# Kernel optimization log

Measured on AMD Instinct MI355X. Metric: run time of the kernel, lower is better.

The kernel has to match this reference:

```python
import jax, jax.numpy as jnp
import numpy as np

K = 20
EPS = 1e-5

def leaky(y):
    return jnp.where(y > 0, y, 0.2 * y)

def knn(x, k):
    # x: [B, C, N] -> idx [B, N, k] of nearest neighbors (incl. self)
    xx = jnp.sum(x * x, axis=1)                      # [B, N]
    inner = jnp.einsum('bcn,bcm->bnm', x, x)          # [B, N, N]
    pd = -xx[:, :, None] + 2.0 * inner - xx[:, None, :]  # negative sq dist
    return jax.lax.top_k(pd, k)[1]

def get_graph_feature(x, k):
    # x: [B, C, N] -> [B, 2C, N, k]
    idx = knn(x, k)
    xt = jnp.transpose(x, (0, 2, 1))                  # [B, N, C]
    feat = jax.vmap(lambda xb, ib: xb[ib])(xt, idx)   # [B, N, k, C]
    center = xt[:, :, None, :]
    out = jnp.concatenate([feat - center, jnp.broadcast_to(center, feat.shape)], axis=-1)
    return jnp.transpose(out, (0, 3, 1, 2))

def bn(y, g, b, axes, shape):
    m = jnp.mean(y, axis=axes, keepdims=True)
    v = jnp.var(y, axis=axes, keepdims=True)
    return (y - m) * jax.lax.rsqrt(v + EPS) * g.reshape(shape) + b.reshape(shape)

def edge_block(x, W, g, b, k):
    f = get_graph_feature(x, k)                       # [B, 2C, N, k]
    y = jnp.einsum('bcnk,oc->bonk', f, W)             # 1x1 conv2d, no bias
    y = leaky(bn(y, g, b, (0, 2, 3), (1, -1, 1, 1)))
    return jnp.max(y, axis=-1)                        # [B, O, N]

def setup_inputs():
    key = jax.random.key(0)
    ks = jax.random.split(key, 8)
    d = {
        'x':  jax.random.normal(ks[0], (16, 3, 2048), jnp.float32),
        'W1': jax.random.normal(ks[1], (64, 6), jnp.float32) * 0.1,
        'g1': jnp.ones((64,)), 'b1': jnp.zeros((64,)),
        'W2': jax.random.normal(ks[2], (64, 128), jnp.float32) * 0.1,
        'g2': jnp.ones((64,)), 'b2': jnp.zeros((64,)),
        'W3': jax.random.normal(ks[3], (128, 128), jnp.float32) * 0.1,
        'g3': jnp.ones((128,)), 'b3': jnp.zeros((128,)),
        'W4': jax.random.normal(ks[4], (256, 256), jnp.float32) * 0.1,
        'g4': jnp.ones((256,)), 'b4': jnp.zeros((256,)),
        'W5': jax.random.normal(ks[5], (1024, 512), jnp.float32) * 0.05,
        'g5': jnp.ones((1024,)), 'b5': jnp.zeros((1024,)),
        'Wl': jax.random.normal(ks[6], (256, 2048), jnp.float32) * 0.02,
        'g6': jnp.ones((256,)), 'b6': jnp.zeros((256,)),
    }
    return d

def reference(x, W1, g1, b1, W2, g2, b2, W3, g3, b3, W4, g4, b4, W5, g5, b5, Wl, g6, b6):
    x1 = edge_block(x,  W1, g1, b1, K)   # [B, 64, N]
    x2 = edge_block(x1, W2, g2, b2, K)   # [B, 64, N]
    x3 = edge_block(x2, W3, g3, b3, K)   # [B, 128, N]
    x4 = edge_block(x3, W4, g4, b4, K)   # [B, 256, N]
    h = jnp.concatenate([x1, x2, x3, x4], axis=1)       # [B, 512, N]
    y = jnp.einsum('bcn,oc->bon', h, W5)                 # 1x1 conv1d
    y = leaky(bn(y, g5, b5, (0, 2), (1, -1, 1)))         # [B, 1024, N]
    p = jnp.concatenate([jnp.max(y, axis=-1), jnp.mean(y, axis=-1)], axis=1)  # [B, 2048]
    z = p @ Wl.T                                          # [B, 256]
    return bn(z, g6, b6, (0,), (1, -1))
```

## Files before the change

kernel.cpp:

```cpp
#include <hip/hip_runtime.h>
#include <float.h>
#include <math.h>

#define BB 16
#define NN 2048
#define KNNK 20
#define HC 512
#define O5 1024
#define EPSF 1e-5f
#define GBLK 2048

__device__ __forceinline__ float leakyf(float y){ return y > 0.f ? y : 0.2f*y; }

__device__ __forceinline__ void bsort_step(float& v, int& id, int lane, int k, int j){
  float pv = __shfl_xor(v, j, 64);
  int pid = __shfl_xor(id, j, 64);
  bool up = ((lane & k) == 0);
  bool iLow = ((lane & j) == 0);
  bool pBefore = (pv > v) || (pv == v && pid < id);
  if ((up == iLow) ? pBefore : !pBefore){ v = pv; id = pid; }
}

__global__ void k_transpose(const float* __restrict__ x, float* __restrict__ xP){
  int gid = blockIdx.x*256 + threadIdx.x;
  if (gid >= BB*NN) return;
  int b = gid / NN, n = gid % NN;
  const float* xb = x + (size_t)b*3*NN;
  *(float4*)&xP[(size_t)gid*4] = make_float4(xb[n], xb[NN + n], xb[2*NN + n], 0.f);
}

__global__ void k_sqn(const float* __restrict__ xin, int xs, int C, float* __restrict__ sqn){
  int gid = blockIdx.x*256 + threadIdx.x;
  if (gid >= BB*NN) return;
  const float* r = xin + (size_t)gid*xs;
  float s = 0.f;
  for (int c = 0; c < C; ++c){ float v = r[c]; s = fmaf(v, v, s); }
  sqn[gid] = s;
}

template<int C, bool WARM>
__global__ __launch_bounds__(256) void k_knn(const float* __restrict__ xin, int xs,
                                             const float* __restrict__ sqn,
                                             const int* __restrict__ idx_prev,
                                             int* __restrict__ idx_out){
  const int TN = 16, MC = 256;
  __shared__ float xnT[WARM ? 1 : 8][20];
  __shared__ float xmT[(C == 3 ? 1 : 16)][MC + 4];
  __shared__ float cval[TN][24];
  __shared__ int   cidx[TN][24];
  __shared__ float sqnn[TN];
  int tid = threadIdx.x;
  int b = (blockIdx.x*TN) / NN, n0 = (blockIdx.x*TN) % NN;
  const float* xb = xin + (size_t)b*NN*xs;

  if constexpr (!WARM){
    for (int e = tid; e < TN*C; e += 256){
      int r = e / C, c = e % C;
      xnT[c][r] = xb[(size_t)(n0+r)*xs + c];
    }
  }
  if (tid < TN) sqnn[tid] = sqn[b*NN + n0 + tid];
  __syncthreads();

  int wid = tid >> 6, lane = tid & 63, r0 = wid*4;
  float tv[4]; int ti[4];

  int urow[4];
  #pragma unroll
  for (int i = 0; i < 4; ++i) urow[i] = __builtin_amdgcn_readfirstlane(n0 + r0 + i);

  if constexpr (WARM){
    #pragma unroll
    for (int i = 0; i < 4; ++i){
      int r = r0 + i;
      int m = (lane < KNNK) ? idx_prev[(size_t)(b*NN + n0 + r)*KNNK + lane] : 0;
      const float* xq = xb + (size_t)urow[i]*xs;
      const float* xm = xb + (size_t)m*xs;
      float dot = 0.f;
      #pragma unroll 8
      for (int c = 0; c < C; c += 4){
        float4 qv = *(const float4*)(xq + c);
        float4 mv = *(const float4*)(xm + c);
        dot = fmaf(qv.x, mv.x, dot);
        dot = fmaf(qv.y, mv.y, dot);
        dot = fmaf(qv.z, mv.z, dot);
        dot = fmaf(qv.w, mv.w, dot);
      }
      float dval = (lane < KNNK) ? ((2.f*dot - sqnn[r]) - sqn[b*NN + m]) : -FLT_MAX;
      int did = (lane < KNNK) ? m : 0x7fffffff;
      #pragma unroll
      for (int k = 2; k <= 64; k <<= 1)
        #pragma unroll
        for (int jj = k >> 1; jj > 0; jj >>= 1)
          bsort_step(dval, did, lane, k, jj);
      if (lane < KNNK){ cval[r][lane] = dval; cidx[r][lane] = did; }
      tv[i] = __shfl(dval, KNNK-1); ti[i] = __shfl(did, KNNK-1);
    }
    __syncthreads();
  }

  for (int base = 0; base < NN; base += MC){
    float pd[4][4];
    if constexpr (C == 3){
      int m0g = base + lane*4;
      const float* xm = xb + (size_t)m0g*4;
      float4 q0 = *(const float4*)&xm[0];
      float4 q1 = *(const float4*)&xm[4];
      float4 q2 = *(const float4*)&xm[8];
      float4 q3 = *(const float4*)&xm[12];
      float4 sm4 = *(const float4*)&sqn[b*NN + m0g];
      #pragma unroll
      for (int i = 0; i < 4; ++i){
        float a0 = xnT[0][r0+i], a1 = xnT[1][r0+i], a2 = xnT[2][r0+i], sq = sqnn[r0+i];
        float d0 = a0*q0.x; d0 = fmaf(a1, q0.y, d0); d0 = fmaf(a2, q0.z, d0);
        float d1 = a0*q1.x; d1 = fmaf(a1, q1.y, d1); d1 = fmaf(a2, q1.z, d1);
        float d2 = a0*q2.x; d2 = fmaf(a1, q2.y, d2); d2 = fmaf(a2, q2.z, d2);
        float d3 = a0*q3.x; d3 = fmaf(a1, q3.y, d3); d3 = fmaf(a2, q3.z, d3);
        pd[i][0] = (2.f*d0 - sq) - sm4.x;
        pd[i][1] = (2.f*d1 - sq) - sm4.y;
        pd[i][2] = (2.f*d2 - sq) - sm4.z;
        pd[i][3] = (2.f*d3 - sq) - sm4.w;
      }
    } else {
      float acc[4][4] = {};
      const float* xq0 = xb + (size_t)urow[0]*xs;
      const float* xq1 = xb + (size_t)urow[1]*xs;
      const float* xq2 = xb + (size_t)urow[2]*xs;
      const float* xq3 = xb + (size_t)urow[3]*xs;
      int pm = tid >> 2, fq = tid & 3;
      for (int c0 = 0; c0 < C; c0 += 16){
        #pragma unroll
        for (int p = 0; p < 4; ++p){
          int pt = p*64 + pm;
          float4 vv = *(const float4*)(xb + (size_t)(base + pt)*xs + c0 + fq*4);
          xmT[fq*4+0][pt] = vv.x; xmT[fq*4+1][pt] = vv.y;
          xmT[fq*4+2][pt] = vv.z; xmT[fq*4+3][pt] = vv.w;
        }
        __syncthreads();
        #pragma unroll
        for (int cc4 = 0; cc4 < 16; cc4 += 4){
          float aq[4][4];
          *(float4*)&aq[0][0] = *(const float4*)(xq0 + c0 + cc4);
          *(float4*)&aq[1][0] = *(const float4*)(xq1 + c0 + cc4);
          *(float4*)&aq[2][0] = *(const float4*)(xq2 + c0 + cc4);
          *(float4*)&aq[3][0] = *(const float4*)(xq3 + c0 + cc4);
          #pragma unroll
          for (int dc = 0; dc < 4; ++dc){
            float4 m4 = *(const float4*)&xmT[cc4+dc][lane*4];
            float mv[4] = {m4.x, m4.y, m4.z, m4.w};
            #pragma unroll
            for (int i = 0; i < 4; ++i)
              #pragma unroll
              for (int p = 0; p < 4; ++p)
                acc[i][p] = fmaf(aq[i][dc], mv[p], acc[i][p]);
          }
        }
        __syncthreads();
      }
      float4 sm4 = *(const float4*)&sqn[b*NN + base + lane*4];
      float smr[4] = {sm4.x, sm4.y, sm4.z, sm4.w};
      #pragma unroll
      for (int i = 0; i < 4; ++i){
        float sq = sqnn[r0+i];
        #pragma unroll
        for (int j = 0; j < 4; ++j)
          pd[i][j] = (2.f*acc[i][j] - sq) - smr[j];
      }
    }

    bool handled = false;
    if constexpr (!WARM){
      if (base == 0){
        handled = true;
        float lv[4]; int li[4];
        #pragma unroll
        for (int i = 0; i < 4; ++i){
          float v0 = pd[i][0]; int j0 = 0;
          if (pd[i][1] > v0){ v0 = pd[i][1]; j0 = 1; }
          if (pd[i][2] > v0){ v0 = pd[i][2]; j0 = 2; }
          if (pd[i][3] > v0){ v0 = pd[i][3]; j0 = 3; }
          lv[i] = v0; li[i] = lane*4 + j0;
        }
        float bv[4]; int bi[4];
        for (int it = 0; it < KNNK; ++it){
          #pragma unroll
          for (int i = 0; i < 4; ++i){ bv[i] = lv[i]; bi[i] = li[i]; }
          #pragma unroll
          for (int off = 1; off < 64; off <<= 1){
            #pragma unroll
            for (int i = 0; i < 4; ++i){
              float ov = __shfl_xor(bv[i], off, 64);
              int oi = __shfl_xor(bi[i], off, 64);
              if (ov > bv[i] || (ov == bv[i] && oi < bi[i])){ bv[i] = ov; bi[i] = oi; }
            }
          }
          #pragma unroll
          for (int i = 0; i < 4; ++i){
            if (lane == it){ cval[r0+i][it] = bv[i]; cidx[r0+i][it] = bi[i]; }
            int wl = bi[i] >> 2, wj = bi[i] & 3;
            if (lane == wl){
              pd[i][0] = (wj == 0) ? -FLT_MAX : pd[i][0];
              pd[i][1] = (wj == 1) ? -FLT_MAX : pd[i][1];
              pd[i][2] = (wj == 2) ? -FLT_MAX : pd[i][2];
              pd[i][3] = (wj == 3) ? -FLT_MAX : pd[i][3];
              float v0 = pd[i][0]; int j0 = 0;
              if (pd[i][1] > v0){ v0 = pd[i][1]; j0 = 1; }
              if (pd[i][2] > v0){ v0 = pd[i][2]; j0 = 2; }
              if (pd[i][3] > v0){ v0 = pd[i][3]; j0 = 3; }
              lv[i] = v0; li[i] = lane*4 + j0;
            }
          }
        }
        #pragma unroll
        for (int i = 0; i < 4; ++i){ tv[i] = bv[i]; ti[i] = bi[i]; }
      }
    }
    if (!handled){
      #pragma unroll
      for (int i = 0; i < 4; ++i){
        int r = r0 + i;
        bool pred = false;
        #pragma unroll
        for (int j = 0; j < 4; ++j){
          int ci = base + lane*4 + j;
          pred = pred || (pd[i][j] > tv[i]) || (pd[i][j] == tv[i] && ci < ti[i]);
        }
        unsigned long long mask = __ballot(pred);
        while (mask){
          int l = __builtin_ctzll(mask); mask &= (mask - 1);
          float cv0 = __shfl(pd[i][0], l);
          float cv1 = __shfl(pd[i][1], l);
          float cv2 = __shfl(pd[i][2], l);
          float cv3 = __shfl(pd[i][3], l);
          #pragma unroll
          for (int j = 0; j < 4; ++j){
            float cv = (j == 0) ? cv0 : (j == 1) ? cv1 : (j == 2) ? cv2 : cv3;
            int ci = base + l*4 + j;
            if (cv > tv[i] || (cv == tv[i] && ci < ti[i])){
              bool skip = false;
              if constexpr (WARM){
                skip = __ballot((lane < KNNK) && (cidx[r][lane] == ci)) != 0ull;
              }
              if (!skip){
                float ev = -FLT_MAX; int ei = 0x7fffffff;
                if (lane < KNNK){ ev = cval[r][lane]; ei = cidx[r][lane]; }
                bool ahead = (lane < KNNK) && (ev > cv || (ev == cv && ei < ci));
                int pos = __popcll(__ballot(ahead));
                float pev = __shfl_up(ev, 1);
                int   pei = __shfl_up(ei, 1);
                float nv; int ni;
                if (lane < pos){ nv = ev; ni = ei; }
                else if (lane == pos){ nv = cv; ni = ci; }
                else { nv = pev; ni = pei; }
                if (lane < KNNK){ cval[r][lane] = nv; cidx[r][lane] = ni; }
                tv[i] = __shfl(nv, 19); ti[i] = __shfl(ni, 19);
              }
            }
          }
        }
      }
    }
  }

  if (lane < KNNK){
    #pragma unroll
    for (int i = 0; i < 4; ++i){
      int r = r0 + i;
      idx_out[(size_t)(b*NN + n0 + r)*KNNK + lane] = cidx[r][lane];
    }
  }
}

__global__ void k_wprep(const float* __restrict__ W, int O, int C,
                        float* __restrict__ wu, float* __restrict__ wv){
  int i = blockIdx.x*256 + threadIdx.x;
  if (i >= O*C) return;
  int o = i / C, c = i % C;
  float a = W[(size_t)o*2*C + c], b = W[(size_t)o*2*C + C + c];
  wu[i] = a; wv[i] = b - a;
}

__global__ __launch_bounds__(256) void k_uv(const float* __restrict__ xin, int xs, int C,
                                            const float* __restrict__ wu, const float* __restrict__ wv,
                                            int O, float* __restrict__ u, float* __restrict__ v){
  __shared__ float xsh[16][68];
  __shared__ float wush[16][68], wvsh[16][68];
  int tid = threadIdx.x;
  int rb = blockIdx.x*64, ob = blockIdx.y*64;
  int otx = tid % 16, rty = tid / 16;
  float au[4][4] = {}, av[4][4] = {};
  for (int c0 = 0; c0 < C; c0 += 16){
    #pragma unroll
    for (int i = 0; i < 4; ++i){
      int c = otx, r = rty*4 + i;
      xsh[c][r]  = (c0 + c < C) ? xin[(size_t)(rb+r)*xs + c0 + c] : 0.f;
      wush[c][r] = (c0 + c < C) ? wu[(size_t)(ob+r)*C + c0 + c] : 0.f;
      wvsh[c][r] = (c0 + c < C) ? wv[(size_t)(ob+r)*C + c0 + c] : 0.f;
    }
    __syncthreads();
    #pragma unroll
    for (int c = 0; c < 16; ++c){
      float4 xr = *(const float4*)&xsh[c][rty*4];
      float4 wa = *(const float4*)&wush[c][otx*4];
      float4 wb = *(const float4*)&wvsh[c][otx*4];
      float xv[4] = {xr.x, xr.y, xr.z, xr.w};
      float wav[4] = {wa.x, wa.y, wa.z, wa.w};
      float wbv[4] = {wb.x, wb.y, wb.z, wb.w};
      #pragma unroll
      for (int i = 0; i < 4; ++i)
        #pragma unroll
        for (int j = 0; j < 4; ++j){
          au[i][j] = fmaf(xv[i], wav[j], au[i][j]);
          av[i][j] = fmaf(xv[i], wbv[j], av[i][j]);
        }
    }
    __syncthreads();
  }
  #pragma unroll
  for (int i = 0; i < 4; ++i){
    size_t r = (size_t)(rb + rty*4 + i);
    *(float4*)&u[r*O + ob + otx*4] = make_float4(au[i][0], au[i][1], au[i][2], au[i][3]);
    *(float4*)&v[r*O + ob + otx*4] = make_float4(av[i][0], av[i][1], av[i][2], av[i][3]);
  }
}

__global__ __launch_bounds__(256) void k_gather(const float* __restrict__ u, const float* __restrict__ v,
                                                const int* __restrict__ idx, int O,
                                                float* __restrict__ s,
                                                float* __restrict__ gp1, float* __restrict__ gp2){
  __shared__ float r1[256], r2[256];
  int tid = threadIdx.x;
  int Ppar = 256 / O;
  int o = tid % O, g = tid / O;
  int p0 = blockIdx.x*16;
  float cs = 0.f, cs2 = 0.f;
  int IT = 16 / Ppar;
  for (int it = 0; it < IT; ++it){
    int pi = p0 + it*Ppar + g;
    int b = pi / NN;
    const int* il = idx + (size_t)pi*KNNK;
    float vv = v[(size_t)pi*O + o];
    float mx = -FLT_MAX, su = 0.f, su2 = 0.f;
    #pragma unroll
    for (int k = 0; k < KNNK; ++k){
      int m = il[k];
      float um = u[((size_t)b*NN + m)*O + o];
      mx = fmaxf(mx, um); su += um; su2 = fmaf(um, um, su2);
    }
    s[(size_t)pi*O + o] = mx + vv;
    cs += su + (float)KNNK*vv;
    cs2 += su2 + 2.f*vv*su + (float)KNNK*vv*vv;
  }
  r1[tid] = cs; r2[tid] = cs2;
  __syncthreads();
  if (tid < O){
    float t1 = 0.f, t2 = 0.f;
    for (int gg = 0; gg < Ppar; ++gg){ t1 += r1[gg*O + tid]; t2 += r2[gg*O + tid]; }
    gp1[(size_t)tid*GBLK + blockIdx.x] = t1;
    gp2[(size_t)tid*GBLK + blockIdx.x] = t2;
  }
}

__global__ __launch_bounds__(256) void k_pred(const float* __restrict__ gp1, const float* __restrict__ gp2,
                                              float* __restrict__ S1, float* __restrict__ S2){
  __shared__ float r1[256], r2[256];
  int o = blockIdx.x, t = threadIdx.x;
  float a = 0.f, b = 0.f;
  #pragma unroll
  for (int i = 0; i < GBLK/256; ++i){
    a += gp1[(size_t)o*GBLK + i*256 + t];
    b += gp2[(size_t)o*GBLK + i*256 + t];
  }
  r1[t] = a; r2[t] = b;
  __syncthreads();
  for (int off = 128; off > 0; off >>= 1){
    if (t < off){ r1[t] += r1[t + off]; r2[t] += r2[t + off]; }
    __syncthreads();
  }
  if (t == 0){ S1[o] = r1[0]; S2[o] = r2[0]; }
}

__global__ void k_fin(const float* __restrict__ S1, const float* __restrict__ S2,
                      const float* __restrict__ g, const float* __restrict__ bb,
                      int O, float cnt, float* __restrict__ A, float* __restrict__ Bp){
  int o = blockIdx.x*256 + threadIdx.x;
  if (o >= O) return;
  float m = S1[o] / cnt;
  float var = S2[o] / cnt - m*m;
  float sc = g[o] / sqrtf(var + EPSF);
  A[o] = sc; Bp[o] = bb[o] - m*sc;
}

__global__ void k_bnle(const float* __restrict__ s, const float* __restrict__ A,
                       const float* __restrict__ Bp, int O, int choff, float* __restrict__ h){
  int gid = blockIdx.x*256 + threadIdx.x;
  int row = gid / O, o = gid % O;
  h[(size_t)row*HC + choff + o] = leakyf(fmaf(s[gid], A[o], Bp[o]));
}

__global__ void k_colsum(const float* __restrict__ hh, float* __restrict__ cp){
  __shared__ float red[4][64];
  int c = threadIdx.x & 63, g = threadIdx.x >> 6;
  int cb = blockIdx.x*64;
  int rbase = blockIdx.y*2048;
  float sacc = 0.f;
  for (int r = rbase + g; r < rbase + 2048; r += 4)
    sacc += hh[(size_t)r*HC + cb + c];
  red[g][c] = sacc;
  __syncthreads();
  if (threadIdx.x < 64){
    float t = red[0][c] + red[1][c] + red[2][c] + red[3][c];
    cp[(size_t)blockIdx.y*HC + cb + c] = t;
  }
}

__global__ void k_csred(const float* __restrict__ cp, float* __restrict__ cs){
  int c = blockIdx.x*256 + threadIdx.x;
  if (c >= HC) return;
  float s = 0.f;
  for (int g = 0; g < 16; ++g) s += cp[(size_t)g*HC + c];
  cs[c] = s;
}

__global__ __launch_bounds__(256) void k_syrk(const float* __restrict__ hh, float* __restrict__ Gp){
  __shared__ float as[16][132], bs[16][132];
  int tid = threadIdx.x;
  int ib = blockIdx.x*128, jb = blockIdx.y*128;
  int k0 = blockIdx.z*1024;
  int cx = tid & 15, ry = tid >> 4;
  int skk = tid >> 4, scc = (tid & 15)*8;
  float acc[8][8] = {};
  for (int kk0 = k0; kk0 < k0 + 1024; kk0 += 16){
    {
      const float* ra = &hh[(size_t)(kk0 + skk)*HC + ib + scc];
      const float* rb2 = &hh[(size_t)(kk0 + skk)*HC + jb + scc];
      float4 a0 = *(const float4*)ra, a1 = *(const float4*)(ra + 4);
      float4 b0 = *(const float4*)rb2, b1 = *(const float4*)(rb2 + 4);
      *(float4*)&as[skk][scc] = a0; *(float4*)&as[skk][scc+4] = a1;
      *(float4*)&bs[skk][scc] = b0; *(float4*)&bs[skk][scc+4] = b1;
    }
    __syncthreads();
    #pragma unroll
    for (int kk = 0; kk < 16; ++kk){
      float4 a0 = *(const float4*)&as[kk][ry*8];
      float4 a1 = *(const float4*)&as[kk][ry*8+4];
      float4 b0 = *(const float4*)&bs[kk][cx*8];
      float4 b1 = *(const float4*)&bs[kk][cx*8+4];
      float av[8] = {a0.x,a0.y,a0.z,a0.w,a1.x,a1.y,a1.z,a1.w};
      float bv[8] = {b0.x,b0.y,b0.z,b0.w,b1.x,b1.y,b1.z,b1.w};
      #pragma unroll
      for (int i = 0; i < 8; ++i)
        #pragma unroll
        for (int j = 0; j < 8; ++j)
          acc[i][j] = fmaf(av[i], bv[j], acc[i][j]);
    }
    __syncthreads();
  }
  float* gz = Gp + (size_t)blockIdx.z*HC*HC;
  #pragma unroll
  for (int i = 0; i < 8; ++i){
    size_t row = (size_t)(ib + ry*8 + i);
    *(float4*)&gz[row*HC + jb + cx*8]     = make_float4(acc[i][0], acc[i][1], acc[i][2], acc[i][3]);
    *(float4*)&gz[row*HC + jb + cx*8 + 4] = make_float4(acc[i][4], acc[i][5], acc[i][6], acc[i][7]);
  }
}

__global__ void k_gred(const float* __restrict__ Gp, float* __restrict__ G){
  int e = blockIdx.x*256 + threadIdx.x;
  float s = 0.f;
  for (int z = 0; z < 32; ++z) s += Gp[(size_t)z*HC*HC + e];
  G[e] = s;
}

__global__ __launch_bounds__(256) void k_quad(const float* __restrict__ G, const float* __restrict__ W5,
                                              const float* __restrict__ cs,
                                              float* __restrict__ S1, float* __restrict__ S2){
  __shared__ float wsh[512];
  __shared__ float red[256];
  int o = blockIdx.x, tid = threadIdx.x;
  for (int j = tid; j < 512; j += 256) wsh[j] = W5[(size_t)o*HC + j];
  __syncthreads();
  float q = 0.f;
  for (int i = tid; i < 512; i += 256){
    float wi = wsh[i];
    float rd = 0.f;
    for (int j = 0; j < 512; j += 4){
      float4 gv = *(const float4*)&G[(size_t)i*HC + j];
      rd = fmaf(gv.x, wsh[j], rd); rd = fmaf(gv.y, wsh[j+1], rd);
      rd = fmaf(gv.z, wsh[j+2], rd); rd = fmaf(gv.w, wsh[j+3], rd);
    }
    q = fmaf(wi, rd, q);
  }
  float m = 0.f;
  for (int j = tid; j < 512; j += 256) m = fmaf(wsh[j], cs[j], m);
  red[tid] = q; __syncthreads();
  for (int off = 128; off > 0; off >>= 1){ if (tid < off) red[tid] += red[tid + off]; __syncthreads(); }
  if (tid == 0) S2[o] = red[0];
  __syncthreads();
  red[tid] = m; __syncthreads();
  for (int off = 128; off > 0; off >>= 1){ if (tid < off) red[tid] += red[tid + off]; __syncthreads(); }
  if (tid == 0) S1[o] = red[0];
}

__global__ __launch_bounds__(256) void k_gemm5b(const float* __restrict__ hh, const float* __restrict__ W5,
                                                const float* __restrict__ A, const float* __restrict__ Bp,
                                                float* __restrict__ mpart, float* __restrict__ spart){
  __shared__ float hs[16][132];
  __shared__ float ws[16][132];
  int tid = threadIdx.x;
  int rb = blockIdx.x*128, ob = blockIdx.y*128;
  int cx = tid & 15, ry = tid >> 4;
  float acc[8][8] = {};
  for (int c0 = 0; c0 < 512; c0 += 16){
    int rr = tid & 127, q0 = (tid >> 7)*4;
    #pragma unroll
    for (int qq = 0; qq < 2; ++qq){
      int kk = q0 + qq*8;
      float4 hv = *(const float4*)&hh[(size_t)(rb+rr)*HC + c0 + kk];
      hs[kk+0][rr] = hv.x; hs[kk+1][rr] = hv.y; hs[kk+2][rr] = hv.z; hs[kk+3][rr] = hv.w;
      float4 wv = *(const float4*)&W5[(size_t)(ob+rr)*HC + c0 + kk];
      ws[kk+0][rr] = wv.x; ws[kk+1][rr] = wv.y; ws[kk+2][rr] = wv.z; ws[kk+3][rr] = wv.w;
    }
    __syncthreads();
    #pragma unroll
    for (int kk = 0; kk < 16; ++kk){
      float4 a0 = *(const float4*)&hs[kk][ry*8];
      float4 a1 = *(const float4*)&hs[kk][ry*8+4];
      float4 b0 = *(const float4*)&ws[kk][cx*8];
      float4 b1 = *(const float4*)&ws[kk][cx*8+4];
      float av[8] = {a0.x,a0.y,a0.z,a0.w,a1.x,a1.y,a1.z,a1.w};
      float bv[8] = {b0.x,b0.y,b0.z,b0.w,b1.x,b1.y,b1.z,b1.w};
      #pragma unroll
      for (int i = 0; i < 8; ++i)
        #pragma unroll
        for (int j = 0; j < 8; ++j)
          acc[i][j] = fmaf(av[i], bv[j], acc[i][j]);
    }
    __syncthreads();
  }
  float Ao[8], Bo[8];
  #pragma unroll
  for (int j = 0; j < 8; ++j){ Ao[j] = A[ob + cx*8 + j]; Bo[j] = Bp[ob + cx*8 + j]; }
  float cmx[8], csm[8];
  #pragma unroll
  for (int j = 0; j < 8; ++j){ cmx[j] = -FLT_MAX; csm[j] = 0.f; }
  #pragma unroll
  for (int i = 0; i < 8; ++i)
    #pragma unroll
    for (int j = 0; j < 8; ++j){
      float a = leakyf(fmaf(acc[i][j], Ao[j], Bo[j]));
      cmx[j] = fmaxf(cmx[j], a); csm[j] += a;
    }
  __syncthreads();
  #pragma unroll
  for (int j = 0; j < 8; ++j){ hs[ry][cx*8 + j] = cmx[j]; ws[ry][cx*8 + j] = csm[j]; }
  __syncthreads();
  if (tid < 128){
    float mx = -FLT_MAX, sm = 0.f;
    for (int g = 0; g < 16; ++g){ mx = fmaxf(mx, hs[g][tid]); sm += ws[g][tid]; }
    int bbi = rb / NN, ntile = (rb % NN) >> 7;
    int o = ob + tid;
    mpart[((size_t)bbi*O5 + o)*16 + ntile] = mx;
    spart[((size_t)bbi*O5 + o)*16 + ntile] = sm;
  }
}

__global__ void k_pool(const float* __restrict__ mpart, const float* __restrict__ spart,
                       float* __restrict__ p){
  int gid = blockIdx.x*256 + threadIdx.x;
  if (gid >= BB*O5) return;
  int b = gid / O5, o = gid % O5;
  const float* mp = mpart + (size_t)(b*O5 + o)*16;
  const float* sp = spart + (size_t)(b*O5 + o)*16;
  float mx = -FLT_MAX, sm = 0.f;
  for (int t = 0; t < 16; ++t){ mx = fmaxf(mx, mp[t]); sm += sp[t]; }
  p[(size_t)b*2048 + o] = mx;
  p[(size_t)b*2048 + 1024 + o] = sm * (1.f/2048.f);
}

__global__ __launch_bounds__(256) void k_final(const float* __restrict__ p, const float* __restrict__ Wl,
                                               const float* __restrict__ g6, const float* __restrict__ b6,
                                               float* __restrict__ out){
  __shared__ float red[16][257];
  int oc = blockIdx.x, tid = threadIdx.x;
  float acc[16] = {};
  for (int j = tid; j < 2048; j += 256){
    float w = Wl[(size_t)oc*2048 + j];
    #pragma unroll
    for (int b = 0; b < 16; ++b) acc[b] = fmaf(p[(size_t)b*2048 + j], w, acc[b]);
  }
  #pragma unroll
  for (int b = 0; b < 16; ++b) red[b][tid] = acc[b];
  __syncthreads();
  for (int off = 128; off > 0; off >>= 1){
    if (tid < off){
      #pragma unroll
      for (int b = 0; b < 16; ++b) red[b][tid] += red[b][tid + off];
    }
    __syncthreads();
  }
  if (tid == 0){
    float m = 0.f;
    for (int b = 0; b < 16; ++b) m += red[b][0];
    m *= (1.f/16.f);
    float var = 0.f;
    for (int b = 0; b < 16; ++b){ float d = red[b][0] - m; var = fmaf(d, d, var); }
    var *= (1.f/16.f);
    float sc = g6[oc] / sqrtf(var + EPSF);
    for (int b = 0; b < 16; ++b) out[(size_t)b*256 + oc] = (red[b][0] - m)*sc + b6[oc];
  }
}

extern "C" void kernel_launch(void* const* d_in, const int* in_sizes, int n_in,
                              void* d_out, int out_size, void* d_ws, size_t ws_size,
                              hipStream_t stream){
  const float* x  = (const float*)d_in[0];
  const float* W1 = (const float*)d_in[1];  const float* g1 = (const float*)d_in[2];  const float* b1 = (const float*)d_in[3];
  const float* W2 = (const float*)d_in[4];  const float* g2 = (const float*)d_in[5];  const float* b2 = (const float*)d_in[6];
  const float* W3 = (const float*)d_in[7];  const float* g3 = (const float*)d_in[8];  const float* b3 = (const float*)d_in[9];
  const float* W4 = (const float*)d_in[10]; const float* g4 = (const float*)d_in[11]; const float* b4 = (const float*)d_in[12];
  const float* W5 = (const float*)d_in[13]; const float* g5 = (const float*)d_in[14]; const float* b5 = (const float*)d_in[15];
  const float* Wl = (const float*)d_in[16]; const float* g6 = (const float*)d_in[17]; const float* b6 = (const float*)d_in[18];
  float* out = (float*)d_out;

  float* ws = (float*)d_ws;
  size_t off = 0;
  auto alloc = [&](size_t n){ float* pp = ws + off; off += n; return pp; };
  float* h    = alloc((size_t)BB*NN*HC);
  float* u    = alloc((size_t)BB*NN*256);
  float* v    = alloc((size_t)BB*NN*256);
  float* s    = alloc((size_t)BB*NN*256);
  float* xP   = alloc((size_t)BB*NN*4);
  float* sqn  = alloc((size_t)BB*NN);
  int*   idxA = (int*)alloc((size_t)BB*NN*KNNK);
  int*   idxB = (int*)alloc((size_t)BB*NN*KNNK);
  float* wu   = alloc(256*128);
  float* wv   = alloc(256*128);
  float* S1   = alloc(1024);
  float* S2   = alloc(1024);
  float* Ab   = alloc(1024);
  float* Bb   = alloc(1024);
  float* mpart= alloc((size_t)BB*O5*16);
  float* spart= alloc((size_t)BB*O5*16);
  float* pbuf = alloc((size_t)BB*2048);
  float* G    = alloc((size_t)HC*HC);
  float* cs   = alloc(HC);
  float* cp   = alloc((size_t)16*HC);
  float* gp1  = alloc((size_t)256*GBLK);
  float* gp2  = alloc((size_t)256*GBLK);
  float* Gp   = u;

  k_transpose<<<(BB*NN)/256, 256, 0, stream>>>(x, xP);

  struct Cfg { const float* xin; int xs, C, O, choff; const float* W; const float* g; const float* bb; };
  Cfg cfg[4] = {
    { xP,    4,   3,   64,   0, W1, g1, b1 },
    { h,     HC,  64,  64,  64, W2, g2, b2 },
    { h+64,  HC,  64, 128, 128, W3, g3, b3 },
    { h+128, HC, 128, 256, 256, W4, g4, b4 },
  };

  int* cur = idxA;
  int* prv = idxB;
  for (int i = 0; i < 4; ++i){
    const Cfg& c = cfg[i];
    k_sqn<<<(BB*NN)/256, 256, 0, stream>>>(c.xin, c.xs, c.C, sqn);
    if (i == 0)           k_knn<3,false><<<(BB*NN)/16, 256, 0, stream>>>(c.xin, c.xs, sqn, nullptr, cur);
    else if (c.C == 64)   k_knn<64,true><<<(BB*NN)/16, 256, 0, stream>>>(c.xin, c.xs, sqn, prv, cur);
    else                  k_knn<128,true><<<(BB*NN)/16, 256, 0, stream>>>(c.xin, c.xs, sqn, prv, cur);
    int OC = c.O * c.C;
    k_wprep<<<(OC + 255)/256, 256, 0, stream>>>(c.W, c.O, c.C, wu, wv);
    k_uv<<<dim3((BB*NN)/64, c.O/64), 256, 0, stream>>>(c.xin, c.xs, c.C, wu, wv, c.O, u, v);
    k_gather<<<GBLK, 256, 0, stream>>>(u, v, cur, c.O, s, gp1, gp2);
    k_pred<<<c.O, 256, 0, stream>>>(gp1, gp2, S1, S2);
    k_fin<<<4, 256, 0, stream>>>(S1, S2, c.g, c.bb, c.O, (float)((size_t)BB*NN*KNNK), Ab, Bb);
    k_bnle<<<((size_t)BB*NN*c.O)/256, 256, 0, stream>>>(s, Ab, Bb, c.O, c.choff, h);
    int* t = cur; cur = prv; prv = t;
  }

  k_colsum<<<dim3(8, 16), 256, 0, stream>>>(h, cp);
  k_csred<<<2, 256, 0, stream>>>(cp, cs);
  k_syrk<<<dim3(4, 4, 32), 256, 0, stream>>>(h, Gp);
  k_gred<<<(HC*HC)/256, 256, 0, stream>>>(Gp, G);
  k_quad<<<O5, 256, 0, stream>>>(G, W5, cs, S1, S2);
  k_fin<<<4, 256, 0, stream>>>(S1, S2, g5, b5, O5, (float)((size_t)BB*NN), Ab, Bb);
  k_gemm5b<<<dim3((BB*NN)/128, O5/128), 256, 0, stream>>>(h, W5, Ab, Bb, mpart, spart);
  k_pool<<<(BB*O5)/256, 256, 0, stream>>>(mpart, spart, pbuf);

  k_final<<<256, 256, 0, stream>>>(pbuf, Wl, g6, b6, out);
}
```

Before: 2.445 ms.

## Run final conv1d GEMM on bf16 MFMA with fused BN/leaky/pool epilogue

New measurement: 2.134 ms. 12.7% less time.

```diff
diff --git a/kernel.cpp b/kernel.cpp
--- a/kernel.cpp
+++ b/kernel.cpp
@@ -10,7 +10,16 @@
 #define EPSF 1e-5f
 #define GBLK 2048
 
+typedef short bf16x8 __attribute__((ext_vector_type(8)));
+typedef float f32x4 __attribute__((ext_vector_type(4)));
+
 __device__ __forceinline__ float leakyf(float y){ return y > 0.f ? y : 0.2f*y; }
+
+__device__ __forceinline__ ushort f2bf(float f){
+  unsigned u = __float_as_uint(f);
+  unsigned r = (u + 0x7fffu + ((u >> 16) & 1u)) >> 16;
+  return (ushort)r;
+}
 
 __device__ __forceinline__ void bsort_step(float& v, int& id, int lane, int k, int j){
   float pv = __shfl_xor(v, j, 64);
@@ -398,6 +407,22 @@
   h[(size_t)row*HC + choff + o] = leakyf(fmaf(s[gid], A[o], Bp[o]));
 }
 
+__global__ void k_h2bf(const float* __restrict__ h, ushort* __restrict__ hbf){
+  int gid = blockIdx.x*256 + threadIdx.x;
+  float4 v = *(const float4*)&h[(size_t)gid*4];
+  ushort4 o;
+  o.x = f2bf(v.x); o.y = f2bf(v.y); o.z = f2bf(v.z); o.w = f2bf(v.w);
+  *(ushort4*)&hbf[(size_t)gid*4] = o;
+}
+
+__global__ void k_w5cvt(const float* __restrict__ W5, ushort* __restrict__ w5bf){
+  int gid = blockIdx.x*256 + threadIdx.x;
+  float4 v = *(const float4*)&W5[(size_t)gid*4];
+  ushort4 o;
+  o.x = f2bf(v.x); o.y = f2bf(v.y); o.z = f2bf(v.z); o.w = f2bf(v.w);
+  *(ushort4*)&w5bf[(size_t)gid*4] = o;
+}
+
 __global__ void k_colsum(const float* __restrict__ hh, float* __restrict__ cp){
   __shared__ float red[4][64];
   int c = threadIdx.x & 63, g = threadIdx.x >> 6;
@@ -502,66 +527,80 @@
   if (tid == 0) S1[o] = red[0];
 }
 
-__global__ __launch_bounds__(256) void k_gemm5b(const float* __restrict__ hh, const float* __restrict__ W5,
+__global__ __launch_bounds__(256) void k_gemm5m(const ushort* __restrict__ hbf, const ushort* __restrict__ w5bf,
                                                 const float* __restrict__ A, const float* __restrict__ Bp,
                                                 float* __restrict__ mpart, float* __restrict__ spart){
-  __shared__ float hs[16][132];
-  __shared__ float ws[16][132];
+  __shared__ ushort lh[128][40];
+  __shared__ ushort lw[128][40];
+  __shared__ float redm[4][128], reds[4][128];
   int tid = threadIdx.x;
   int rb = blockIdx.x*128, ob = blockIdx.y*128;
-  int cx = tid & 15, ry = tid >> 4;
-  float acc[8][8] = {};
-  for (int c0 = 0; c0 < 512; c0 += 16){
-    int rr = tid & 127, q0 = (tid >> 7)*4;
-    #pragma unroll
-    for (int qq = 0; qq < 2; ++qq){
-      int kk = q0 + qq*8;
-      float4 hv = *(const float4*)&hh[(size_t)(rb+rr)*HC + c0 + kk];
-      hs[kk+0][rr] = hv.x; hs[kk+1][rr] = hv.y; hs[kk+2][rr] = hv.z; hs[kk+3][rr] = hv.w;
-      float4 wv = *(const float4*)&W5[(size_t)(ob+rr)*HC + c0 + kk];
-      ws[kk+0][rr] = wv.x; ws[kk+1][rr] = wv.y; ws[kk+2][rr] = wv.z; ws[kk+3][rr] = wv.w;
-    }
-    __syncthreads();
-    #pragma unroll
-    for (int kk = 0; kk < 16; ++kk){
-      float4 a0 = *(const float4*)&hs[kk][ry*8];
-      float4 a1 = *(const float4*)&hs[kk][ry*8+4];
-      float4 b0 = *(const float4*)&ws[kk][cx*8];
-      float4 b1 = *(const float4*)&ws[kk][cx*8+4];
-      float av[8] = {a0.x,a0.y,a0.z,a0.w,a1.x,a1.y,a1.z,a1.w};
-      float bv[8] = {b0.x,b0.y,b0.z,b0.w,b1.x,b1.y,b1.z,b1.w};
+  int wid = tid >> 6, lane = tid & 63;
+  int lrow = lane & 15, lk = lane >> 4;
+  f32x4 acc[2][8];
+  #pragma unroll
+  for (int i = 0; i < 2; ++i)
+    #pragma unroll
+    for (int j = 0; j < 8; ++j)
+      acc[i][j] = (f32x4){0.f, 0.f, 0.f, 0.f};
+  int srow = tid >> 1, shalf = tid & 1;
+  for (int kt = 0; kt < 16; ++kt){
+    int k0 = kt*32;
+    const uint4* gh = (const uint4*)&hbf[(size_t)(rb+srow)*HC + k0 + shalf*16];
+    uint4 v0 = gh[0], v1 = gh[1];
+    const uint4* gw = (const uint4*)&w5bf[(size_t)(ob+srow)*HC + k0 + shalf*16];
+    uint4 w0 = gw[0], w1 = gw[1];
+    __syncthreads();
+    *(uint4*)&lh[srow][shalf*16]     = v0;
+    *(uint4*)&lh[srow][shalf*16 + 8] = v1;
+    *(uint4*)&lw[srow][shalf*16]     = w0;
+    *(uint4*)&lw[srow][shalf*16 + 8] = w1;
+    __syncthreads();
+    bf16x8 afr0 = *(const bf16x8*)&lh[wid*32 + lrow][lk*8];
+    bf16x8 afr1 = *(const bf16x8*)&lh[wid*32 + 16 + lrow][lk*8];
+    #pragma unroll
+    for (int ct = 0; ct < 8; ++ct){
+      bf16x8 bfr = *(const bf16x8*)&lw[ct*16 + lrow][lk*8];
+      acc[0][ct] = __builtin_amdgcn_mfma_f32_16x16x32_bf16(afr0, bfr, acc[0][ct], 0, 0, 0);
+      acc[1][ct] = __builtin_amdgcn_mfma_f32_16x16x32_bf16(afr1, bfr, acc[1][ct], 0, 0, 0);
+    }
+  }
+  float mx[8], sm[8];
+  #pragma unroll
+  for (int ct = 0; ct < 8; ++ct){
+    int o = ob + ct*16 + lrow;
+    float Ao = A[o], Bo = Bp[o];
+    float m = -FLT_MAX, s = 0.f;
+    #pragma unroll
+    for (int tA = 0; tA < 2; ++tA)
       #pragma unroll
-      for (int i = 0; i < 8; ++i)
-        #pragma unroll
-        for (int j = 0; j < 8; ++j)
-          acc[i][j] = fmaf(av[i], bv[j], acc[i][j]);
-    }
-    __syncthreads();
-  }
-  float Ao[8], Bo[8];
-  #pragma unroll
-  for (int j = 0; j < 8; ++j){ Ao[j] = A[ob + cx*8 + j]; Bo[j] = Bp[ob + cx*8 + j]; }
-  float cmx[8], csm[8];
-  #pragma unroll
-  for (int j = 0; j < 8; ++j){ cmx[j] = -FLT_MAX; csm[j] = 0.f; }
-  #pragma unroll
-  for (int i = 0; i < 8; ++i)
-    #pragma unroll
-    for (int j = 0; j < 8; ++j){
-      float a = leakyf(fmaf(acc[i][j], Ao[j], Bo[j]));
-      cmx[j] = fmaxf(cmx[j], a); csm[j] += a;
-    }
-  __syncthreads();
-  #pragma unroll
-  for (int j = 0; j < 8; ++j){ hs[ry][cx*8 + j] = cmx[j]; ws[ry][cx*8 + j] = csm[j]; }
+      for (int q = 0; q < 4; ++q){
+        float y = leakyf(fmaf(acc[tA][ct][q], Ao, Bo));
+        m = fmaxf(m, y); s += y;
+      }
+    #pragma unroll
+    for (int off = 16; off < 64; off <<= 1){
+      m = fmaxf(m, __shfl_xor(m, off, 64));
+      s += __shfl_xor(s, off, 64);
+    }
+    mx[ct] = m; sm[ct] = s;
+  }
+  __syncthreads();
+  if (lane < 16){
+    #pragma unroll
+    for (int ct = 0; ct < 8; ++ct){
+      redm[wid][ct*16 + lane] = mx[ct];
+      reds[wid][ct*16 + lane] = sm[ct];
+    }
+  }
   __syncthreads();
   if (tid < 128){
-    float mx = -FLT_MAX, sm = 0.f;
-    for (int g = 0; g < 16; ++g){ mx = fmaxf(mx, hs[g][tid]); sm += ws[g][tid]; }
+    float m = fmaxf(fmaxf(redm[0][tid], redm[1][tid]), fmaxf(redm[2][tid], redm[3][tid]));
+    float s = reds[0][tid] + reds[1][tid] + reds[2][tid] + reds[3][tid];
     int bbi = rb / NN, ntile = (rb % NN) >> 7;
     int o = ob + tid;
-    mpart[((size_t)bbi*O5 + o)*16 + ntile] = mx;
-    spart[((size_t)bbi*O5 + o)*16 + ntile] = sm;
+    mpart[((size_t)bbi*O5 + o)*16 + ntile] = m;
+    spart[((size_t)bbi*O5 + o)*16 + ntile] = s;
   }
 }
 
@@ -648,7 +687,9 @@
   float* cp   = alloc((size_t)16*HC);
   float* gp1  = alloc((size_t)256*GBLK);
   float* gp2  = alloc((size_t)256*GBLK);
+  ushort* w5bf = (ushort*)alloc(262144);
   float* Gp   = u;
+  ushort* hbf = (ushort*)s;
 
   k_transpose<<<(BB*NN)/256, 256, 0, stream>>>(x, xP);
 
@@ -678,13 +719,16 @@
     int* t = cur; cur = prv; prv = t;
   }
 
+  k_h2bf<<<((size_t)BB*NN*HC)/(256*4), 256, 0, stream>>>(h, hbf);
+  k_w5cvt<<<((size_t)O5*HC)/(256*4), 256, 0, stream>>>(W5, w5bf);
+
   k_colsum<<<dim3(8, 16), 256, 0, stream>>>(h, cp);
   k_csred<<<2, 256, 0, stream>>>(cp, cs);
   k_syrk<<<dim3(4, 4, 32), 256, 0, stream>>>(h, Gp);
   k_gred<<<(HC*HC)/256, 256, 0, stream>>>(Gp, G);
   k_quad<<<O5, 256, 0, stream>>>(G, W5, cs, S1, S2);
   k_fin<<<4, 256, 0, stream>>>(S1, S2, g5, b5, O5, (float)((size_t)BB*NN), Ab, Bb);
-  k_gemm5b<<<dim3((BB*NN)/128, O5/128), 256, 0, stream>>>(h, W5, Ab, Bb, mpart, spart);
+  k_gemm5m<<<dim3((BB*NN)/128, O5/128), 256, 0, stream>>>(hbf, w5bf, Ab, Bb, mpart, spart);
   k_pool<<<(BB*O5)/256, 256, 0, stream>>>(mpart, spart, pbuf);
 
   k_final<<<256, 256, 0, stream>>>(pbuf, Wl, g6, b6, out);
```
